# Optimization experiments

Hardware: AMD Instinct MI355X
Metric: run time of the kernel (lower is better)

## Reference

```python
import jax, jax.numpy as jnp
import numpy as np

T, B, H, K = 512, 64, 512, 16  # seq_len, batch, hidden_size, num_tags


def setup_inputs() -> dict:
    key = jax.random.key(0)
    ks = jax.random.split(key, 8)
    hidden = jax.random.normal(ks[0], (T, B, H), dtype=jnp.float32)
    W1 = jax.random.normal(ks[1], (H, H), dtype=jnp.float32) / np.float32(np.sqrt(H))
    b1 = jnp.zeros((H,), jnp.float32)
    W2 = jax.random.normal(ks[2], (H, K), dtype=jnp.float32) / np.float32(np.sqrt(H))
    b2 = jnp.zeros((K,), jnp.float32)
    transition = jax.random.normal(ks[3], (K, K), dtype=jnp.float32)
    lens = jax.random.randint(ks[4], (B,), T // 2, T + 1)  # valid lengths in [T/2, T]
    tags = jax.random.randint(ks[5], (T, B), 0, K)
    return dict(hidden=hidden, W1=W1, b1=b1, W2=W2, b2=b2,
                transition=transition, lens=lens, tags=tags)


def reference(hidden, W1, b1, W2, b2, transition, lens, tags):
    # Emission MLP (dropout is identity in eval): Linear -> ReLU -> Linear
    h = jax.nn.relu(hidden @ W1 + b1)          # [T, B, H]
    em = h @ W2 + b2                           # [T, B, K]

    # ---- forward (partition) score: linear-chain logsumexp DP ----
    def step(alpha, e_t):
        # alpha: [B, K] over prev tags; transition[curr, prev]
        a = jax.nn.logsumexp(alpha[:, None, :] + transition[None, :, :], axis=-1) + e_t
        return a, a

    alpha0 = em[0]
    _, alphas = jax.lax.scan(step, alpha0, em[1:])
    alphas = jnp.concatenate([alpha0[None], alphas], axis=0)            # [T, B, K]
    last = jnp.take_along_axis(alphas, (lens - 1)[None, :, None], axis=0)[0]  # [B, K]
    fwd_score = jax.nn.logsumexp(last, axis=-1)                          # [B]

    # ---- gold path score ----
    em_path = jnp.take_along_axis(em, tags[:, :, None], axis=-1)[..., 0]  # [T, B]
    trans_path = transition[tags[1:], tags[:-1]]                          # [T-1, B]
    steps = em_path.at[1:].add(trans_path)
    cum = jnp.cumsum(steps, axis=0)                                       # [T, B]
    gold = jnp.take_along_axis(cum, (lens - 1)[None, :], axis=0)[0]       # [B]

    return (fwd_score - gold).sum()
```

## Files before the change

kernel.cpp:

```cpp
#include <hip/hip_runtime.h>
#include <hip/hip_bf16.h>

#define TT 512
#define BB 64
#define HH 512
#define KK 16

#define NCH 32
#define CST (TT / NCH)

typedef __attribute__((ext_vector_type(8))) short bf16x8;
typedef __attribute__((ext_vector_type(4))) short bf16x4;
typedef __attribute__((ext_vector_type(4))) float f32x4;

#define MFMA_K16(A, B, C) __builtin_amdgcn_mfma_f32_16x16x16bf16_1k(A, B, C, 0, 0, 0)

__device__ __forceinline__ unsigned short f2bf(float f) {
    union { __hip_bfloat16 h; unsigned short u; } cvt;
    cvt.h = __float2bfloat16(f);
    return cvt.u;
}

__device__ __forceinline__ short rne_bf(float x) {
    unsigned u = __float_as_uint(x);
    u += 0x7fffu + ((u >> 16) & 1u);
    return (short)(u >> 16);
}

__device__ __forceinline__ float bf2f(short s) {
    return __uint_as_float(((unsigned)(unsigned short)s) << 16);
}

__global__ void prep_kernel(const float* __restrict__ W1, const float* __restrict__ W2,
                            unsigned short* __restrict__ W1t, unsigned short* __restrict__ W2t,
                            float* __restrict__ out) {
    const int bi = blockIdx.x, tx = threadIdx.x;
    if (bi < 64) {
        __shared__ float Ls[64][65];
        const int ti = bi & 7, tj = bi >> 3;
        const int r0 = ti * 64, c0 = tj * 64;
        const int r = tx >> 4, c4 = (tx & 15) * 4;
#pragma unroll
        for (int i = 0; i < 4; ++i) {
            float4 v = *(const float4*)(W1 + (size_t)(r0 + r + 16 * i) * HH + c0 + c4);
            Ls[c4 + 0][r + 16 * i] = v.x;
            Ls[c4 + 1][r + 16 * i] = v.y;
            Ls[c4 + 2][r + 16 * i] = v.z;
            Ls[c4 + 3][r + 16 * i] = v.w;
        }
        __syncthreads();
        const int rn = tx >> 4, k4 = (tx & 15) * 4;
#pragma unroll
        for (int i = 0; i < 4; ++i) {
            const int n = rn + 16 * i;
            ushort4 o;
            o.x = f2bf(Ls[n][k4 + 0]);
            o.y = f2bf(Ls[n][k4 + 1]);
            o.z = f2bf(Ls[n][k4 + 2]);
            o.w = f2bf(Ls[n][k4 + 3]);
            *(ushort4*)(W1t + (size_t)(c0 + n) * HH + r0 + k4) = o;
        }
    } else {
        if (tx == 0) out[0] = 0.0f;
        for (int idx = tx; idx < 16 * HH; idx += 256) {
            const int n = idx >> 9, k = idx & 511;
            W2t[idx] = f2bf(W2[k * KK + n]);
        }
    }
}

__global__ __launch_bounds__(256, 4)
void em_kernel(const float* __restrict__ hidden, const unsigned short* __restrict__ W1t,
               const float* __restrict__ b1, const unsigned short* __restrict__ W2t,
               const float* __restrict__ b2, float* __restrict__ em) {
    __shared__ __align__(16) unsigned char stage[35328];
    unsigned short* const As = (unsigned short*)stage;
    unsigned short* const Bs = (unsigned short*)(stage + 2560);

    const int tx = threadIdx.x;
    const int w = tx >> 6, lane = tx & 63;
    const int q = lane >> 4, nl = lane & 15;
    const int row0 = blockIdx.x * 32;
    const int ar = tx >> 3, ac4 = (tx & 7) * 4;

    f32x4 acc[2][8];
#pragma unroll
    for (int mt = 0; mt < 2; ++mt)
#pragma unroll
        for (int nt = 0; nt < 8; ++nt) acc[mt][nt] = (f32x4){0.f, 0.f, 0.f, 0.f};

    for (int kt = 0; kt < 16; ++kt) {
        const int k0 = kt * 32;
        __syncthreads();
#pragma unroll
        for (int it = 0; it < 8; ++it) {
            const int c = it * 256 + tx;
            const int n = c >> 2, slot = c & 3;
            const int kc = slot ^ ((n >> 1) & 3);
            __builtin_amdgcn_global_load_lds(
                (const __attribute__((address_space(1))) void*)(W1t + (size_t)n * HH + k0 + kc * 8),
                (__attribute__((address_space(3))) void*)(Bs + c * 8), 16, 0, 0);
        }
        {
            float4 v = *(const float4*)(hidden + (size_t)(row0 + ar) * HH + k0 + ac4);
            ushort4 o;
            o.x = f2bf(v.x); o.y = f2bf(v.y);
            o.z = f2bf(v.z); o.w = f2bf(v.w);
            *(ushort4*)(As + ar * 40 + ac4) = o;
        }
        __syncthreads();
        bf16x8 af[2];
#pragma unroll
        for (int mt = 0; mt < 2; ++mt)
            af[mt] = *(const bf16x8*)(As + (16 * mt + nl) * 40 + q * 8);
#pragma unroll
        for (int nt = 0; nt < 8; ++nt) {
            const int n = 128 * w + 16 * nt + nl;
            const int slot = q ^ ((n >> 1) & 3);
            bf16x8 bf = *(const bf16x8*)(Bs + n * 32 + slot * 8);
            acc[0][nt] = __builtin_amdgcn_mfma_f32_16x16x32_bf16(af[0], bf, acc[0][nt], 0, 0, 0);
            acc[1][nt] = __builtin_amdgcn_mfma_f32_16x16x32_bf16(af[1], bf, acc[1][nt], 0, 0, 0);
        }
    }

    __syncthreads();
    unsigned short* const W2s = (unsigned short*)stage;
    unsigned short* const Hb  = (unsigned short*)(stage + 16640);
#pragma unroll
    for (int i = tx; i < 1024; i += 256) {
        const int n = i >> 6, kc = i & 63;
        *(bf16x8*)(W2s + n * 520 + kc * 8) = *(const bf16x8*)(W2t + n * HH + kc * 8);
    }
#pragma unroll
    for (int nt = 0; nt < 8; ++nt) {
        const float bv = b1[128 * w + 16 * nt + nl];
#pragma unroll
        for (int mt = 0; mt < 2; ++mt) {
#pragma unroll
            for (int r = 0; r < 4; ++r) {
                float v = acc[mt][nt][r] + bv;
                v = v > 0.f ? v : 0.f;
                Hb[(16 * mt + q * 4 + r) * 264 + 128 * w + 16 * nt + nl] = f2bf(v);
            }
        }
    }
    __syncthreads();
    if (w < 2) {
        f32x4 acc2 = (f32x4){0.f, 0.f, 0.f, 0.f};
#pragma unroll
        for (int ks = 0; ks < 16; ++ks) {
            bf16x8 a2  = *(const bf16x8*)(Hb + (16 * w + nl) * 264 + ks * 32 + q * 8);
            bf16x8 b2f = *(const bf16x8*)(W2s + nl * 520 + ks * 32 + q * 8);
            acc2 = __builtin_amdgcn_mfma_f32_16x16x32_bf16(a2, b2f, acc2, 0, 0, 0);
        }
#pragma unroll
        for (int r = 0; r < 4; ++r) {
            const int row = row0 + 16 * w + q * 4 + r;
            em[(size_t)row * KK + nl] = acc2[r] + b2[nl];
        }
    }
}

__global__ void gold_kernel(const float* __restrict__ em, const float* __restrict__ trans,
                            const int* __restrict__ lens, const int* __restrict__ tags,
                            float* __restrict__ out) {
    __shared__ float trs[256];
    __shared__ float red[4];
    const int tid = threadIdx.x;
    trs[tid] = __logf(bf2f(rne_bf(__expf(trans[tid]))));
    __syncthreads();
    const int idx = blockIdx.x * 256 + tid;
    const int t = idx >> 6, b = idx & 63;
    const int L = lens[b];
    float v = 0.0f;
    if (t < L) {
        const int tg = tags[t * BB + b];
        v = em[((size_t)t * BB + b) * KK + tg];
        if (t > 0) v += trs[tg * 16 + tags[(t - 1) * BB + b]];
    }
#pragma unroll
    for (int dd = 1; dd < 64; dd <<= 1) v += __shfl_xor(v, dd, 64);
    if ((tid & 63) == 0) red[tid >> 6] = v;
    __syncthreads();
    if (tid == 0) atomicAdd(out, -(red[0] + red[1] + red[2] + red[3]));
}

__global__ void chunk_kernel(const float* __restrict__ em, const float* __restrict__ trans,
                             const int* __restrict__ lens,
                             float* __restrict__ Pfull, float* __restrict__ Cfull,
                             float* __restrict__ Ppart, float* __restrict__ Cpart) {
    const int tx = threadIdx.x;
    const int id = blockIdx.x * 4 + (tx >> 6);
    const int lane = tx & 63, q = lane >> 4, col = lane & 15;
    const int b = id >> 5, c = id & 31;

    float mf[4];
    {
        float4 tv = *(const float4*)(trans + col * 16 + 4 * q);
        mf[0] = bf2f(rne_bf(__expf(tv.x)));
        mf[1] = bf2f(rne_bf(__expf(tv.y)));
        mf[2] = bf2f(rne_bf(__expf(tv.z)));
        mf[3] = bf2f(rne_bf(__expf(tv.w)));
    }
    const int Lm1 = lens[b] - 1;
    const int tb0 = CST * c;

    float ebuf[8];
#pragma unroll
    for (int i = 0; i < 8; ++i)
        ebuf[i] = em[(size_t)((tb0 + i) * BB + b) * KK + col];

    bf16x4 gb;
#pragma unroll
    for (int i = 0; i < 4; ++i)
        gb[i] = (4 * q + i == col) ? rne_bf(1.0f) : (short)0;

    const f32x4 zc = (f32x4){0.f, 0.f, 0.f, 0.f};
    f32x4 d = (f32x4){0.f, 0.f, 0.f, 0.f};
    float K = 1.0f, rk = 1.0f, lk = 0.0f, Cacc = 0.0f;

    for (int sb = 0; sb < CST; sb += 8) {
        const bool refill = (sb < CST - 8);
#pragma unroll
        for (int s8 = 0; s8 < 8; ++s8) {
            const int t = tb0 + sb + s8;
            const float eraw = ebuf[s8];
            if (refill)
                ebuf[s8] = em[(size_t)((t + 8) * BB + b) * KK + col];
            float ev = __expf(eraw);
            if ((s8 & 3) == 0 && (sb + s8) >= 4) {
                ev *= rk;
                Cacc += lk;
            }
            bf16x4 af;
            af[0] = rne_bf(ev * mf[0]); af[1] = rne_bf(ev * mf[1]);
            af[2] = rne_bf(ev * mf[2]); af[3] = rne_bf(ev * mf[3]);
            if (s8 == 0) {
                if (sb == 0 && c == 0) {
#pragma unroll
                    for (int i = 0; i < 4; ++i)
                        af[i] = (4 * q + i == col) ? rne_bf(ev) : (short)0;
                }
            }
            d = MFMA_K16(af, gb, zc);
            if ((s8 & 3) == 1) {
                K = __shfl(d[0], 0, 64);
                const float Km = fmaxf(K, 1e-30f);
                rk = 1.0f / Km;
                lk = __logf(Km);
            }
            if (t == Lm1) {
#pragma unroll
                for (int r = 0; r < 4; ++r)
                    Ppart[b * 256 + (4 * q + r) * 16 + col] = d[r];
                if (lane == 0) Cpart[b] = Cacc;
            }
            gb[0] = rne_bf(d[0]); gb[1] = rne_bf(d[1]);
            gb[2] = rne_bf(d[2]); gb[3] = rne_bf(d[3]);
        }
    }
#pragma unroll
    for (int r = 0; r < 4; ++r)
        Pfull[(size_t)(b * NCH + c) * 256 + (4 * q + r) * 16 + col] = d[r];
    if (lane == 0) Cfull[b * NCH + c] = Cacc;
}

__global__ void combine_kernel(const int* __restrict__ lens,
                               const float* __restrict__ Pfull, const float* __restrict__ Cfull,
                               const float* __restrict__ Ppart, const float* __restrict__ Cpart,
                               float* __restrict__ out) {
    const int lane = threadIdx.x;
    const int grp = lane >> 4, j = lane & 15;
    const int b = blockIdx.x * 4 + grp;
    const int base = grp << 4;
    const int cstar = (lens[b] - 1) / CST;

    float g = 1.0f, acc = 0.0f;
    for (int c = 0; c < NCH; ++c) {
        const bool act = (c <= cstar);
        const float* P = (c < cstar) ? (Pfull + (size_t)(b * NCH + c) * 256)
                                     : (Ppart + b * 256);
        float gn = 0.0f;
#pragma unroll
        for (int k = 0; k < 16; ++k) {
            const float gk = __shfl(g, base + k, 64);
            gn += P[j * 16 + k] * gk;
        }
        if (act) {
            float m = gn;
#pragma unroll
            for (int dd = 1; dd < 16; dd <<= 1) m = fmaxf(m, __shfl_xor(m, dd, 64));
            g = gn / m;
            acc += __logf(m) + ((c < cstar) ? Cfull[b * NCH + c] : Cpart[b]);
        }
    }
    float ssum = g;
#pragma unroll
    for (int dd = 1; dd < 16; dd <<= 1) ssum += __shfl_xor(ssum, dd, 64);
    const float fwd = acc + __logf(ssum);
    if (j == 0) atomicAdd(out, fwd);
}

extern "C" void kernel_launch(void* const* d_in, const int* in_sizes, int n_in,
                              void* d_out, int out_size, void* d_ws, size_t ws_size,
                              hipStream_t stream) {
    const float* hidden = (const float*)d_in[0];
    const float* W1     = (const float*)d_in[1];
    const float* b1     = (const float*)d_in[2];
    const float* W2     = (const float*)d_in[3];
    const float* b2     = (const float*)d_in[4];
    const float* trans  = (const float*)d_in[5];
    const int*   lens   = (const int*)d_in[6];
    const int*   tags   = (const int*)d_in[7];
    float* out = (float*)d_out;

    char* ws = (char*)d_ws;
    float* em = (float*)ws;
    unsigned short* W1t = (unsigned short*)(ws + 2097152);
    unsigned short* W2t = (unsigned short*)(ws + 2621440);
    float* Pfull = (float*)(ws + 2637824);
    float* Cfull = (float*)(ws + 4734976);
    float* Ppart = (float*)(ws + 4743168);
    float* Cpart = (float*)(ws + 4808704);

    prep_kernel<<<65, 256, 0, stream>>>(W1, W2, W1t, W2t, out);
    em_kernel<<<1024, 256, 0, stream>>>(hidden, W1t, b1, W2t, b2, em);
    gold_kernel<<<128, 256, 0, stream>>>(em, trans, lens, tags, out);
    chunk_kernel<<<512, 256, 0, stream>>>(em, trans, lens, Pfull, Cfull, Ppart, Cpart);
    combine_kernel<<<16, 64, 0, stream>>>(lens, Pfull, Cfull, Ppart, Cpart, out);
}
```

Baseline: 173.7 us.

## Double em GEMM row tile, merge gold and chunk kernels, halve chunk count

Result: faster. 148.1 us (-14.7%).

```diff
diff --git a/kernel.cpp b/kernel.cpp
--- a/kernel.cpp
+++ b/kernel.cpp
@@ -6,7 +6,7 @@
 #define HH 512
 #define KK 16
 
-#define NCH 32
+#define NCH 16
 #define CST (TT / NCH)
 
 typedef __attribute__((ext_vector_type(8))) short bf16x8;
@@ -69,23 +69,23 @@
     }
 }
 
-__global__ __launch_bounds__(256, 4)
+__global__ __launch_bounds__(256, 2)
 void em_kernel(const float* __restrict__ hidden, const unsigned short* __restrict__ W1t,
                const float* __restrict__ b1, const unsigned short* __restrict__ W2t,
                const float* __restrict__ b2, float* __restrict__ em) {
-    __shared__ __align__(16) unsigned char stage[35328];
+    __shared__ __align__(16) unsigned char stage[50432];
     unsigned short* const As = (unsigned short*)stage;
-    unsigned short* const Bs = (unsigned short*)(stage + 2560);
+    unsigned short* const Bs = (unsigned short*)(stage + 5120);
 
     const int tx = threadIdx.x;
     const int w = tx >> 6, lane = tx & 63;
     const int q = lane >> 4, nl = lane & 15;
-    const int row0 = blockIdx.x * 32;
-    const int ar = tx >> 3, ac4 = (tx & 7) * 4;
-
-    f32x4 acc[2][8];
-#pragma unroll
-    for (int mt = 0; mt < 2; ++mt)
+    const int row0 = blockIdx.x * 64;
+    const int ar = tx >> 2, ac8 = (tx & 3) * 8;
+
+    f32x4 acc[4][8];
+#pragma unroll
+    for (int mt = 0; mt < 4; ++mt)
 #pragma unroll
         for (int nt = 0; nt < 8; ++nt) acc[mt][nt] = (f32x4){0.f, 0.f, 0.f, 0.f};
 
@@ -102,97 +102,107 @@
                 (__attribute__((address_space(3))) void*)(Bs + c * 8), 16, 0, 0);
         }
         {
-            float4 v = *(const float4*)(hidden + (size_t)(row0 + ar) * HH + k0 + ac4);
-            ushort4 o;
-            o.x = f2bf(v.x); o.y = f2bf(v.y);
-            o.z = f2bf(v.z); o.w = f2bf(v.w);
-            *(ushort4*)(As + ar * 40 + ac4) = o;
-        }
-        __syncthreads();
-        bf16x8 af[2];
-#pragma unroll
-        for (int mt = 0; mt < 2; ++mt)
+            const float* src = hidden + (size_t)(row0 + ar) * HH + k0 + ac8;
+            float4 v0 = *(const float4*)(src);
+            float4 v1 = *(const float4*)(src + 4);
+            bf16x8 o;
+            o[0] = (short)f2bf(v0.x); o[1] = (short)f2bf(v0.y);
+            o[2] = (short)f2bf(v0.z); o[3] = (short)f2bf(v0.w);
+            o[4] = (short)f2bf(v1.x); o[5] = (short)f2bf(v1.y);
+            o[6] = (short)f2bf(v1.z); o[7] = (short)f2bf(v1.w);
+            *(bf16x8*)(As + ar * 40 + ac8) = o;
+        }
+        __syncthreads();
+        bf16x8 af[4];
+#pragma unroll
+        for (int mt = 0; mt < 4; ++mt)
             af[mt] = *(const bf16x8*)(As + (16 * mt + nl) * 40 + q * 8);
 #pragma unroll
         for (int nt = 0; nt < 8; ++nt) {
             const int n = 128 * w + 16 * nt + nl;
             const int slot = q ^ ((n >> 1) & 3);
             bf16x8 bf = *(const bf16x8*)(Bs + n * 32 + slot * 8);
-            acc[0][nt] = __builtin_amdgcn_mfma_f32_16x16x32_bf16(af[0], bf, acc[0][nt], 0, 0, 0);
-            acc[1][nt] = __builtin_amdgcn_mfma_f32_16x16x32_bf16(af[1], bf, acc[1][nt], 0, 0, 0);
+#pragma unroll
+            for (int mt = 0; mt < 4; ++mt)
+                acc[mt][nt] = __builtin_amdgcn_mfma_f32_16x16x32_bf16(af[mt], bf, acc[mt][nt], 0, 0, 0);
         }
     }
 
     __syncthreads();
-    unsigned short* const W2s = (unsigned short*)stage;
-    unsigned short* const Hb  = (unsigned short*)(stage + 16640);
+    unsigned short* const Hb  = (unsigned short*)stage;
+    unsigned short* const W2s = (unsigned short*)(stage + 33792);
 #pragma unroll
     for (int i = tx; i < 1024; i += 256) {
         const int n = i >> 6, kc = i & 63;
         *(bf16x8*)(W2s + n * 520 + kc * 8) = *(const bf16x8*)(W2t + n * HH + kc * 8);
     }
-#pragma unroll
-    for (int nt = 0; nt < 8; ++nt) {
-        const float bv = b1[128 * w + 16 * nt + nl];
-#pragma unroll
-        for (int mt = 0; mt < 2; ++mt) {
-#pragma unroll
-            for (int r = 0; r < 4; ++r) {
-                float v = acc[mt][nt][r] + bv;
-                v = v > 0.f ? v : 0.f;
-                Hb[(16 * mt + q * 4 + r) * 264 + 128 * w + 16 * nt + nl] = f2bf(v);
-            }
-        }
-    }
-    __syncthreads();
-    if (w < 2) {
-        f32x4 acc2 = (f32x4){0.f, 0.f, 0.f, 0.f};
-#pragma unroll
-        for (int ks = 0; ks < 16; ++ks) {
+
+    f32x4 acc2 = (f32x4){0.f, 0.f, 0.f, 0.f};
+#pragma unroll
+    for (int c = 0; c < 2; ++c) {
+        if ((w >> 1) == c) {
+#pragma unroll
+            for (int nt = 0; nt < 8; ++nt) {
+                const float bv = b1[128 * w + 16 * nt + nl];
+#pragma unroll
+                for (int mt = 0; mt < 4; ++mt) {
+#pragma unroll
+                    for (int r = 0; r < 4; ++r) {
+                        float v = acc[mt][nt][r] + bv;
+                        v = v > 0.f ? v : 0.f;
+                        Hb[(16 * mt + q * 4 + r) * 264 + 128 * (w & 1) + 16 * nt + nl] = f2bf(v);
+                    }
+                }
+            }
+        }
+        __syncthreads();
+#pragma unroll
+        for (int ks = 0; ks < 8; ++ks) {
             bf16x8 a2  = *(const bf16x8*)(Hb + (16 * w + nl) * 264 + ks * 32 + q * 8);
-            bf16x8 b2f = *(const bf16x8*)(W2s + nl * 520 + ks * 32 + q * 8);
+            bf16x8 b2f = *(const bf16x8*)(W2s + nl * 520 + c * 256 + ks * 32 + q * 8);
             acc2 = __builtin_amdgcn_mfma_f32_16x16x32_bf16(a2, b2f, acc2, 0, 0, 0);
         }
-#pragma unroll
-        for (int r = 0; r < 4; ++r) {
-            const int row = row0 + 16 * w + q * 4 + r;
-            em[(size_t)row * KK + nl] = acc2[r] + b2[nl];
-        }
-    }
-}
-
-__global__ void gold_kernel(const float* __restrict__ em, const float* __restrict__ trans,
-                            const int* __restrict__ lens, const int* __restrict__ tags,
-                            float* __restrict__ out) {
+        __syncthreads();
+    }
+#pragma unroll
+    for (int r = 0; r < 4; ++r) {
+        const int row = row0 + 16 * w + q * 4 + r;
+        em[(size_t)row * KK + nl] = acc2[r] + b2[nl];
+    }
+}
+
+__global__ void scan_gold_kernel(const float* __restrict__ em, const float* __restrict__ trans,
+                                 const int* __restrict__ lens, const int* __restrict__ tags,
+                                 float* __restrict__ Pfull, float* __restrict__ Cfull,
+                                 float* __restrict__ Ppart, float* __restrict__ Cpart,
+                                 float* __restrict__ out) {
     __shared__ float trs[256];
     __shared__ float red[4];
-    const int tid = threadIdx.x;
-    trs[tid] = __logf(bf2f(rne_bf(__expf(trans[tid]))));
-    __syncthreads();
-    const int idx = blockIdx.x * 256 + tid;
-    const int t = idx >> 6, b = idx & 63;
-    const int L = lens[b];
-    float v = 0.0f;
-    if (t < L) {
-        const int tg = tags[t * BB + b];
-        v = em[((size_t)t * BB + b) * KK + tg];
-        if (t > 0) v += trs[tg * 16 + tags[(t - 1) * BB + b]];
-    }
-#pragma unroll
-    for (int dd = 1; dd < 64; dd <<= 1) v += __shfl_xor(v, dd, 64);
-    if ((tid & 63) == 0) red[tid >> 6] = v;
-    __syncthreads();
-    if (tid == 0) atomicAdd(out, -(red[0] + red[1] + red[2] + red[3]));
-}
-
-__global__ void chunk_kernel(const float* __restrict__ em, const float* __restrict__ trans,
-                             const int* __restrict__ lens,
-                             float* __restrict__ Pfull, float* __restrict__ Cfull,
-                             float* __restrict__ Ppart, float* __restrict__ Cpart) {
     const int tx = threadIdx.x;
+
+    if (blockIdx.x >= 256) {
+        trs[tx] = __logf(bf2f(rne_bf(__expf(trans[tx]))));
+        __syncthreads();
+        const int idx = (blockIdx.x - 256) * 256 + tx;
+        const int t = idx >> 6, b = idx & 63;
+        const int L = lens[b];
+        float v = 0.0f;
+        if (t < L) {
+            const int tg = tags[t * BB + b];
+            v = em[((size_t)t * BB + b) * KK + tg];
+            if (t > 0) v += trs[tg * 16 + tags[(t - 1) * BB + b]];
+        }
+#pragma unroll
+        for (int dd = 1; dd < 64; dd <<= 1) v += __shfl_xor(v, dd, 64);
+        if ((tx & 63) == 0) red[tx >> 6] = v;
+        __syncthreads();
+        if (tx == 0) atomicAdd(out, -(red[0] + red[1] + red[2] + red[3]));
+        return;
+    }
+
     const int id = blockIdx.x * 4 + (tx >> 6);
     const int lane = tx & 63, q = lane >> 4, col = lane & 15;
-    const int b = id >> 5, c = id & 31;
+    const int b = id >> 4, c = id & 15;
 
     float mf[4];
     {
@@ -319,13 +329,13 @@
     unsigned short* W1t = (unsigned short*)(ws + 2097152);
     unsigned short* W2t = (unsigned short*)(ws + 2621440);
     float* Pfull = (float*)(ws + 2637824);
-    float* Cfull = (float*)(ws + 4734976);
-    float* Ppart = (float*)(ws + 4743168);
-    float* Cpart = (float*)(ws + 4808704);
+    float* Cfull = (float*)(ws + 3686400);
+    float* Ppart = (float*)(ws + 3690496);
+    float* Cpart = (float*)(ws + 3756032);
 
     prep_kernel<<<65, 256, 0, stream>>>(W1, W2, W1t, W2t, out);
-    em_kernel<<<1024, 256, 0, stream>>>(hidden, W1t, b1, W2t, b2, em);
-    gold_kernel<<<128, 256, 0, stream>>>(em, trans, lens, tags, out);
-    chunk_kernel<<<512, 256, 0, stream>>>(em, trans, lens, Pfull, Cfull, Ppart, Cpart);
+    em_kernel<<<512, 256, 0, stream>>>(hidden, W1t, b1, W2t, b2, em);
+    scan_gold_kernel<<<384, 256, 0, stream>>>(em, trans, lens, tags,
+                                              Pfull, Cfull, Ppart, Cpart, out);
     combine_kernel<<<16, 64, 0, stream>>>(lens, Pfull, Cfull, Ppart, Cpart, out);
 }
```
